# Kernel optimization log

Hardware: AMD Instinct MI355X
Metric: run time of the kernel (lower is better)

## Reference

```python
import jax, jax.numpy as jnp
import numpy as np

TOP_K = 16
NUM_HEADS = 1
EPS = 1e-8  # torch F.cosine_similarity eps


def setup_inputs() -> dict:
    key = jax.random.key(0)
    ks = jax.random.split(key, 8)
    B, N, Dk, Dv = 64, 8192, 256, 256
    return {
        "query": jax.random.normal(ks[0], (B, Dk), jnp.float32),
        "key_memory": jax.random.normal(ks[1], (B, N, Dk), jnp.float32),
        "value_memory": jax.random.normal(ks[2], (B, N, Dv), jnp.float32),
        "iteration": jax.random.randint(ks[3], (B, 1), 0, N),
        "in_proj_w": jax.random.normal(ks[4], (3 * Dv, Dv), jnp.float32) * 0.06,
        "in_proj_b": jnp.zeros((3 * Dv,), jnp.float32),
        "out_proj_w": jax.random.normal(ks[5], (Dv, Dv), jnp.float32) * 0.06,
        "out_proj_b": jnp.zeros((Dv,), jnp.float32),
    }


def _mha(x, in_w, in_b, out_w, out_b):
    # torch nn.MultiheadAttention (batch_first, qkv same embed dim) self-attention
    B, T, E = x.shape
    H = NUM_HEADS
    hd = E // H
    qkv = x @ in_w.T + in_b                      # [B,T,3E]
    q, k, v = jnp.split(qkv, 3, axis=-1)

    def heads(t):
        return t.reshape(B, T, H, hd).transpose(0, 2, 1, 3)  # [B,H,T,hd]

    q, k, v = heads(q), heads(k), heads(v)
    scale = jnp.asarray(1.0 / np.sqrt(hd), x.dtype)
    attn = jax.nn.softmax(jnp.einsum('bhqd,bhkd->bhqk', q, k) * scale, axis=-1)
    o = jnp.einsum('bhqk,bhkd->bhqd', attn, v).transpose(0, 2, 1, 3).reshape(B, T, E)
    return o @ out_w.T + out_b


def reference(query, key_memory, value_memory, iteration,
              in_proj_w, in_proj_b, out_proj_w, out_proj_b):
    B, N, Dv = value_memory.shape
    # memory validity mask: item n is valid iff n <= iteration[b]
    mem_idx = jnp.arange(N)[None, :]                                   # [1,N]
    mask = (mem_idx <= iteration).astype(key_memory.dtype)[..., None]  # [B,N,1]
    km = key_memory * mask
    vm = value_memory * mask

    # masked cosine similarity between each memory key and the query
    num = jnp.einsum('bnd,bd->bn', km, query)                          # [B,N]
    denom = jnp.maximum(
        jnp.linalg.norm(km, axis=-1) * jnp.linalg.norm(query, axis=-1, keepdims=True),
        EPS)
    sim = num / denom                                                  # [B,N]

    topk_sim, topk_idx = jax.lax.top_k(sim, TOP_K)                     # [B,K]
    topk_vm = jnp.take_along_axis(vm, topk_idx[:, :, None], axis=1)    # [B,K,Dv]

    wv = jax.nn.softmax(topk_sim, axis=-1)[..., None]                  # [B,K,1]
    nrv = wv * topk_vm                                                 # [B,K,Dv]

    nrv = _mha(nrv, in_proj_w, in_proj_b, out_proj_w, out_proj_b)      # [B,K,Dv]

    # rows with iteration == 0 are left as zeros (scatter of computed rows)
    not_first = (iteration.reshape(-1) > 0).astype(nrv.dtype)[:, None, None]
    nrv = nrv * not_first
    return nrv.sum(axis=1)                                             # [B,Dv]
```

## Files before the change

### kernel.cpp

```cpp
#include <hip/hip_runtime.h>
#include <hip/hip_bf16.h>
#include <math.h>

#define B_   64
#define N_   8192
#define D_   256
#define K_   16
#define EPS_ 1e-8f
#define NEG_ -3.4e38f

static const size_t CANDV_OFF = 0;
static const size_t CANDI_OFF = 131072;
static const size_t QKV_OFF   = 262144;

__global__ void __launch_bounds__(256)
simtopk_kernel(const float* __restrict__ q, const float* __restrict__ km,
               const int* __restrict__ iter,
               float* __restrict__ cand_v, int* __restrict__ cand_i) {
    int tid  = threadIdx.x;
    int w    = tid >> 6, lane = tid & 63;
    int g    = lane >> 4, p = lane & 15;
    int item = (blockIdx.x << 2) + w;
    int b    = item >> 7;
    int r0   = (item & 127) << 6;
    int it   = iter[b];
    size_t cbase = (size_t)item * K_;

    if (r0 > it) {
        if (lane < K_) { cand_v[cbase + lane] = 0.f; cand_i[cbase + lane] = r0 + lane; }
        return;
    }

    float4 q4[4];
    #pragma unroll
    for (int kk = 0; kk < 4; kk++)
        q4[kk] = *(const float4*)(q + (size_t)b * D_ + kk * 64 + p * 4);
    float qq = 0.f;
    #pragma unroll
    for (int kk = 0; kk < 4; kk++)
        qq += q4[kk].x*q4[kk].x + q4[kk].y*q4[kk].y + q4[kk].z*q4[kk].z + q4[kk].w*q4[kk].w;
    #pragma unroll
    for (int off = 8; off; off >>= 1) qq += __shfl_xor(qq, off);
    float qn = sqrtf(qq);

    float keepv = 0.f;
    const float* kmb = km + (size_t)b * N_ * D_;
    for (int t = 0; t < 8; t++) {
        int ra = r0 + (t << 3) + (g << 1);
        int rb = ra + 1;
        const float* pa = kmb + (size_t)min(ra, it) * D_;
        const float* pb = kmb + (size_t)min(rb, it) * D_;
        float4 ka0 = *(const float4*)(pa +   0 + p * 4);
        float4 ka1 = *(const float4*)(pa +  64 + p * 4);
        float4 ka2 = *(const float4*)(pa + 128 + p * 4);
        float4 ka3 = *(const float4*)(pa + 192 + p * 4);
        float4 kb0 = *(const float4*)(pb +   0 + p * 4);
        float4 kb1 = *(const float4*)(pb +  64 + p * 4);
        float4 kb2 = *(const float4*)(pb + 128 + p * 4);
        float4 kb3 = *(const float4*)(pb + 192 + p * 4);
        float dota = ka0.x*q4[0].x + ka0.y*q4[0].y + ka0.z*q4[0].z + ka0.w*q4[0].w
                   + ka1.x*q4[1].x + ka1.y*q4[1].y + ka1.z*q4[1].z + ka1.w*q4[1].w
                   + ka2.x*q4[2].x + ka2.y*q4[2].y + ka2.z*q4[2].z + ka2.w*q4[2].w
                   + ka3.x*q4[3].x + ka3.y*q4[3].y + ka3.z*q4[3].z + ka3.w*q4[3].w;
        float sqa  = ka0.x*ka0.x + ka0.y*ka0.y + ka0.z*ka0.z + ka0.w*ka0.w
                   + ka1.x*ka1.x + ka1.y*ka1.y + ka1.z*ka1.z + ka1.w*ka1.w
                   + ka2.x*ka2.x + ka2.y*ka2.y + ka2.z*ka2.z + ka2.w*ka2.w
                   + ka3.x*ka3.x + ka3.y*ka3.y + ka3.z*ka3.z + ka3.w*ka3.w;
        float dotb = kb0.x*q4[0].x + kb0.y*q4[0].y + kb0.z*q4[0].z + kb0.w*q4[0].w
                   + kb1.x*q4[1].x + kb1.y*q4[1].y + kb1.z*q4[1].z + kb1.w*q4[1].w
                   + kb2.x*q4[2].x + kb2.y*q4[2].y + kb2.z*q4[2].z + kb2.w*q4[2].w
                   + kb3.x*q4[3].x + kb3.y*q4[3].y + kb3.z*q4[3].z + kb3.w*q4[3].w;
        float sqb  = kb0.x*kb0.x + kb0.y*kb0.y + kb0.z*kb0.z + kb0.w*kb0.w
                   + kb1.x*kb1.x + kb1.y*kb1.y + kb1.z*kb1.z + kb1.w*kb1.w
                   + kb2.x*kb2.x + kb2.y*kb2.y + kb2.z*kb2.z + kb2.w*kb2.w
                   + kb3.x*kb3.x + kb3.y*kb3.y + kb3.z*kb3.z + kb3.w*kb3.w;
        #pragma unroll
        for (int off = 8; off; off >>= 1) {
            dota += __shfl_xor(dota, off);
            sqa  += __shfl_xor(sqa,  off);
            dotb += __shfl_xor(dotb, off);
            sqb  += __shfl_xor(sqb,  off);
        }
        float sa = (ra <= it) ? dota / fmaxf(sqrtf(sqa) * qn, EPS_) : 0.f;
        float sb = (rb <= it) ? dotb / fmaxf(sqrtf(sqb) * qn, EPS_) : 0.f;
        keepv = (p == 2 * t)     ? sa : keepv;
        keepv = (p == 2 * t + 1) ? sb : keepv;
    }
    int keepi = r0 + ((p >> 1) << 3) + (g << 1) + (p & 1);

    #pragma unroll
    for (int k = 2; k <= 64; k <<= 1) {
        #pragma unroll
        for (int j = k >> 1; j > 0; j >>= 1) {
            float pv = __shfl_xor(keepv, j);
            int   pi = __shfl_xor(keepi, j);
            bool up         = ((lane & k) == 0);
            bool is_lower   = ((lane & j) == 0);
            bool mine_first = (keepv > pv) || (keepv == pv && keepi < pi);
            bool take_mine  = ((is_lower == up) == mine_first);
            if (!take_mine) { keepv = pv; keepi = pi; }
        }
    }
    if (lane < K_) { cand_v[cbase + lane] = keepv; cand_i[cbase + lane] = keepi; }
}

__global__ void __launch_bounds__(256)
merge_qkv_kernel(const float* __restrict__ cand_v, const int* __restrict__ cand_i,
                 const float* __restrict__ vm, const int* __restrict__ iter,
                 const float* __restrict__ inw, const float* __restrict__ inb,
                 float* __restrict__ qkv) {
    int bwh = blockIdx.x;
    int b = bwh / 3, which = bwh - b * 3;
    int tid = threadIdx.x, lane = tid & 63;
    int it = iter[b];
    if (it == 0) return;

    __shared__ int   seli[K_];
    __shared__ float selv[K_];
    __shared__ float scl[K_];

    if (tid < 64) {
        float cv[32]; int ci[32];
        #pragma unroll
        for (int j = 0; j < 32; j++) {
            cv[j] = cand_v[(size_t)b * 2048 + (j << 6) + lane];
            ci[j] = cand_i[(size_t)b * 2048 + (j << 6) + lane];
        }
        for (int sel = 0; sel < K_; sel++) {
            float bv = cv[0]; int bi = ci[0];
            #pragma unroll
            for (int j = 1; j < 32; j++)
                if (cv[j] > bv || (cv[j] == bv && ci[j] < bi)) { bv = cv[j]; bi = ci[j]; }
            #pragma unroll
            for (int off = 32; off; off >>= 1) {
                float ov = __shfl_xor(bv, off);
                int   oi = __shfl_xor(bi, off);
                if (ov > bv || (ov == bv && oi < bi)) { bv = ov; bi = oi; }
            }
            #pragma unroll
            for (int j = 0; j < 32; j++)
                if (ci[j] == bi) cv[j] = NEG_;
            if (lane == 0) { selv[sel] = bv; seli[sel] = bi; }
        }
        float m = NEG_;
        #pragma unroll
        for (int jj = 0; jj < K_; jj++) m = fmaxf(m, selv[jj]);
        float ssum = 0.f;
        #pragma unroll
        for (int jj = 0; jj < K_; jj++) ssum += expf(selv[jj] - m);
        if (lane < K_) {
            int row = seli[lane];
            float wgt = expf(selv[lane] - m) / ssum;
            scl[lane] = (row <= it) ? wgt : 0.f;
        }
    }
    __syncthreads();

    float acc[K_];
    #pragma unroll
    for (int k = 0; k < K_; k++) acc[k] = 0.f;
    const float* wrow = inw + (size_t)(which * D_ + tid) * D_;
    for (int blk = 0; blk < 4; blk++) {
        float4 wreg[16];
        #pragma unroll
        for (int u = 0; u < 16; u++)
            wreg[u] = *(const float4*)(wrow + blk * 64 + u * 4);
        #pragma unroll
        for (int k = 0; k < K_; k++) {
            int row = __builtin_amdgcn_readfirstlane(seli[k]);
            const float* vr = vm + ((size_t)b * N_ + row) * D_ + blk * 64;
            float a = 0.f;
            #pragma unroll
            for (int u = 0; u < 16; u++) {
                float4 xv = *(const float4*)(vr + u * 4);
                a += xv.x*wreg[u].x + xv.y*wreg[u].y + xv.z*wreg[u].z + xv.w*wreg[u].w;
            }
            acc[k] += a;
        }
    }
    float bias = inb[which * D_ + tid];
    #pragma unroll
    for (int k = 0; k < K_; k++)
        qkv[(((size_t)b * 3 + which) * K_ + k) * D_ + tid] = scl[k] * acc[k] + bias;
}

__global__ void __launch_bounds__(256)
attn_out_kernel(const float* __restrict__ qkv, const int* __restrict__ iter,
                const float* __restrict__ ow, const float* __restrict__ ob,
                float* __restrict__ out) {
    int b = blockIdx.x, tid = threadIdx.x;
    int it = iter[b];
    if (it == 0) { out[(size_t)b * D_ + tid] = 0.f; return; }
    __shared__ float qs[K_][260];
    __shared__ float ks[K_][260];
    __shared__ float vs[K_][260];
    __shared__ float attn[K_][K_];
    __shared__ float colsum[K_];
    __shared__ float so[D_];
    const float* base = qkv + (size_t)b * 3 * K_ * D_;
    #pragma unroll
    for (int k = 0; k < K_; k++) {
        qs[k][tid] = base[(0 * K_ + k) * D_ + tid];
        ks[k][tid] = base[(1 * K_ + k) * D_ + tid];
        vs[k][tid] = base[(2 * K_ + k) * D_ + tid];
    }
    __syncthreads();
    int i = tid >> 4, j = tid & 15;
    float s = 0.f;
    for (int d4 = 0; d4 < 64; d4++) {
        float4 qv = *(const float4*)(&qs[i][d4 * 4]);
        float4 kv = *(const float4*)(&ks[j][d4 * 4]);
        s += qv.x*kv.x + qv.y*kv.y + qv.z*kv.z + qv.w*kv.w;
    }
    attn[i][j] = s * 0.0625f;
    __syncthreads();
    if (tid < K_) {
        float m = NEG_;
        for (int jj = 0; jj < K_; jj++) m = fmaxf(m, attn[tid][jj]);
        float ssum = 0.f;
        for (int jj = 0; jj < K_; jj++) ssum += expf(attn[tid][jj] - m);
        float inv = 1.f / ssum;
        for (int jj = 0; jj < K_; jj++) attn[tid][jj] = expf(attn[tid][jj] - m) * inv;
    }
    __syncthreads();
    if (tid < K_) {
        float c = 0.f;
        for (int ii = 0; ii < K_; ii++) c += attn[ii][tid];
        colsum[tid] = c;
    }
    __syncthreads();
    float acc = 0.f;
    #pragma unroll
    for (int jj = 0; jj < K_; jj++) acc += colsum[jj] * vs[jj][tid];
    so[tid] = acc;
    __syncthreads();
    float o = 0.f;
    const float* orow = ow + (size_t)tid * D_;
    for (int e = 0; e < D_; e += 4) {
        float4 wv = *(const float4*)(orow + e);
        float4 sv = *(const float4*)(&so[e]);
        o += sv.x*wv.x + sv.y*wv.y + sv.z*wv.z + sv.w*wv.w;
    }
    out[(size_t)b * D_ + tid] = o + 16.f * ob[tid];
}

extern "C" void kernel_launch(void* const* d_in, const int* in_sizes, int n_in,
                              void* d_out, int out_size, void* d_ws, size_t ws_size,
                              hipStream_t stream) {
    const float* q   = (const float*)d_in[0];
    const float* km  = (const float*)d_in[1];
    const float* vm  = (const float*)d_in[2];
    const int*   it  = (const int*)  d_in[3];
    const float* inw = (const float*)d_in[4];
    const float* inb = (const float*)d_in[5];
    const float* ow  = (const float*)d_in[6];
    const float* ob  = (const float*)d_in[7];
    float* out = (float*)d_out;

    float* ws     = (float*)d_ws;
    float* cand_v = ws + CANDV_OFF;
    int*   cand_i = (int*)(ws + CANDI_OFF);
    float* qkv    = ws + QKV_OFF;

    simtopk_kernel<<<dim3(2048), dim3(256), 0, stream>>>(q, km, it, cand_v, cand_i);
    merge_qkv_kernel<<<dim3(B_ * 3), dim3(256), 0, stream>>>(cand_v, cand_i, vm, it, inw, inb, qkv);
    attn_out_kernel<<<dim3(B_), dim3(256), 0, stream>>>(qkv, it, ow, ob, out);
}
```

Before: 158.4 us.

## Split similarity and candidate top-k kernels, prefetch key rows, stage values in LDS

The fused similarity/top-k kernel becomes two kernels. The first computes cosine similarity one row per 16-lane group and software-prefetches the next key row, writing the scores to a workspace buffer. A separate kernel runs the per-segment bitonic sort to pick candidates. The QKV projection now stages the softmax-scaled gathered value rows in shared memory once, so each thread no longer re-reads them from global memory. This adds a kernel launch and a global round-trip of the similarity array, but should reduce redundant value loads and hide key-load latency.

```diff
diff --git a/kernel.cpp b/kernel.cpp
--- a/kernel.cpp
+++ b/kernel.cpp
@@ -9,99 +9,100 @@
 #define EPS_ 1e-8f
 #define NEG_ -3.4e38f
 
-static const size_t CANDV_OFF = 0;
-static const size_t CANDI_OFF = 131072;
-static const size_t QKV_OFF   = 262144;
-
-__global__ void __launch_bounds__(256)
-simtopk_kernel(const float* __restrict__ q, const float* __restrict__ km,
-               const int* __restrict__ iter,
-               float* __restrict__ cand_v, int* __restrict__ cand_i) {
-    int tid  = threadIdx.x;
-    int w    = tid >> 6, lane = tid & 63;
-    int g    = lane >> 4, p = lane & 15;
-    int item = (blockIdx.x << 2) + w;
-    int b    = item >> 7;
-    int r0   = (item & 127) << 6;
-    int it   = iter[b];
-    size_t cbase = (size_t)item * K_;
-
-    if (r0 > it) {
-        if (lane < K_) { cand_v[cbase + lane] = 0.f; cand_i[cbase + lane] = r0 + lane; }
-        return;
-    }
+static const size_t SIM_OFF   = 0;
+static const size_t CANDV_OFF = 524288;
+static const size_t CANDI_OFF = 655360;
+static const size_t QKV_OFF   = 786432;
+
+__global__ void __launch_bounds__(256)
+sim_kernel(const float* __restrict__ q, const float* __restrict__ km,
+           const int* __restrict__ iter, float* __restrict__ sim) {
+    int tid = threadIdx.x;
+    int w = tid >> 6, lane = tid & 63;
+    int g = lane >> 4, p = lane & 15;
+    int seg = (blockIdx.x << 2) + w;
+    int b   = seg >> 7;
+    int n0  = (seg & 127) << 6;
+    int it  = iter[b];
+    float* simb = sim + (size_t)b * N_;
+
+    if (n0 > it) { simb[n0 + lane] = 0.f; return; }
 
     float4 q4[4];
     #pragma unroll
     for (int kk = 0; kk < 4; kk++)
         q4[kk] = *(const float4*)(q + (size_t)b * D_ + kk * 64 + p * 4);
-    float qq = 0.f;
-    #pragma unroll
-    for (int kk = 0; kk < 4; kk++)
-        qq += q4[kk].x*q4[kk].x + q4[kk].y*q4[kk].y + q4[kk].z*q4[kk].z + q4[kk].w*q4[kk].w;
+    float qq = q4[0].x*q4[0].x + q4[0].y*q4[0].y + q4[0].z*q4[0].z + q4[0].w*q4[0].w
+             + q4[1].x*q4[1].x + q4[1].y*q4[1].y + q4[1].z*q4[1].z + q4[1].w*q4[1].w
+             + q4[2].x*q4[2].x + q4[2].y*q4[2].y + q4[2].z*q4[2].z + q4[2].w*q4[2].w
+             + q4[3].x*q4[3].x + q4[3].y*q4[3].y + q4[3].z*q4[3].z + q4[3].w*q4[3].w;
     #pragma unroll
     for (int off = 8; off; off >>= 1) qq += __shfl_xor(qq, off);
     float qn = sqrtf(qq);
 
-    float keepv = 0.f;
     const float* kmb = km + (size_t)b * N_ * D_;
-    for (int t = 0; t < 8; t++) {
-        int ra = r0 + (t << 3) + (g << 1);
-        int rb = ra + 1;
-        const float* pa = kmb + (size_t)min(ra, it) * D_;
-        const float* pb = kmb + (size_t)min(rb, it) * D_;
-        float4 ka0 = *(const float4*)(pa +   0 + p * 4);
-        float4 ka1 = *(const float4*)(pa +  64 + p * 4);
-        float4 ka2 = *(const float4*)(pa + 128 + p * 4);
-        float4 ka3 = *(const float4*)(pa + 192 + p * 4);
-        float4 kb0 = *(const float4*)(pb +   0 + p * 4);
-        float4 kb1 = *(const float4*)(pb +  64 + p * 4);
-        float4 kb2 = *(const float4*)(pb + 128 + p * 4);
-        float4 kb3 = *(const float4*)(pb + 192 + p * 4);
-        float dota = ka0.x*q4[0].x + ka0.y*q4[0].y + ka0.z*q4[0].z + ka0.w*q4[0].w
-                   + ka1.x*q4[1].x + ka1.y*q4[1].y + ka1.z*q4[1].z + ka1.w*q4[1].w
-                   + ka2.x*q4[2].x + ka2.y*q4[2].y + ka2.z*q4[2].z + ka2.w*q4[2].w
-                   + ka3.x*q4[3].x + ka3.y*q4[3].y + ka3.z*q4[3].z + ka3.w*q4[3].w;
-        float sqa  = ka0.x*ka0.x + ka0.y*ka0.y + ka0.z*ka0.z + ka0.w*ka0.w
-                   + ka1.x*ka1.x + ka1.y*ka1.y + ka1.z*ka1.z + ka1.w*ka1.w
-                   + ka2.x*ka2.x + ka2.y*ka2.y + ka2.z*ka2.z + ka2.w*ka2.w
-                   + ka3.x*ka3.x + ka3.y*ka3.y + ka3.z*ka3.z + ka3.w*ka3.w;
-        float dotb = kb0.x*q4[0].x + kb0.y*q4[0].y + kb0.z*q4[0].z + kb0.w*q4[0].w
-                   + kb1.x*q4[1].x + kb1.y*q4[1].y + kb1.z*q4[1].z + kb1.w*q4[1].w
-                   + kb2.x*q4[2].x + kb2.y*q4[2].y + kb2.z*q4[2].z + kb2.w*q4[2].w
-                   + kb3.x*q4[3].x + kb3.y*q4[3].y + kb3.z*q4[3].z + kb3.w*q4[3].w;
-        float sqb  = kb0.x*kb0.x + kb0.y*kb0.y + kb0.z*kb0.z + kb0.w*kb0.w
-                   + kb1.x*kb1.x + kb1.y*kb1.y + kb1.z*kb1.z + kb1.w*kb1.w
-                   + kb2.x*kb2.x + kb2.y*kb2.y + kb2.z*kb2.z + kb2.w*kb2.w
-                   + kb3.x*kb3.x + kb3.y*kb3.y + kb3.z*kb3.z + kb3.w*kb3.w;
+
+    const float* rp0 = kmb + (size_t)min(n0 + g, it) * D_;
+    float4 c0 = *(const float4*)(rp0 +   0 + p * 4);
+    float4 c1 = *(const float4*)(rp0 +  64 + p * 4);
+    float4 c2 = *(const float4*)(rp0 + 128 + p * 4);
+    float4 c3 = *(const float4*)(rp0 + 192 + p * 4);
+
+    for (int t = 0; t < 16; t++) {
+        int r  = n0 + (t << 2) + g;
+        int rn = (t < 15) ? (r + 4) : it;
+        const float* rp = kmb + (size_t)min(rn, it) * D_;
+        float4 x0 = *(const float4*)(rp +   0 + p * 4);
+        float4 x1 = *(const float4*)(rp +  64 + p * 4);
+        float4 x2 = *(const float4*)(rp + 128 + p * 4);
+        float4 x3 = *(const float4*)(rp + 192 + p * 4);
+
+        float dot = c0.x*q4[0].x + c0.y*q4[0].y + c0.z*q4[0].z + c0.w*q4[0].w
+                  + c1.x*q4[1].x + c1.y*q4[1].y + c1.z*q4[1].z + c1.w*q4[1].w
+                  + c2.x*q4[2].x + c2.y*q4[2].y + c2.z*q4[2].z + c2.w*q4[2].w
+                  + c3.x*q4[3].x + c3.y*q4[3].y + c3.z*q4[3].z + c3.w*q4[3].w;
+        float sq  = c0.x*c0.x + c0.y*c0.y + c0.z*c0.z + c0.w*c0.w
+                  + c1.x*c1.x + c1.y*c1.y + c1.z*c1.z + c1.w*c1.w
+                  + c2.x*c2.x + c2.y*c2.y + c2.z*c2.z + c2.w*c2.w
+                  + c3.x*c3.x + c3.y*c3.y + c3.z*c3.z + c3.w*c3.w;
         #pragma unroll
         for (int off = 8; off; off >>= 1) {
-            dota += __shfl_xor(dota, off);
-            sqa  += __shfl_xor(sqa,  off);
-            dotb += __shfl_xor(dotb, off);
-            sqb  += __shfl_xor(sqb,  off);
-        }
-        float sa = (ra <= it) ? dota / fmaxf(sqrtf(sqa) * qn, EPS_) : 0.f;
-        float sb = (rb <= it) ? dotb / fmaxf(sqrtf(sqb) * qn, EPS_) : 0.f;
-        keepv = (p == 2 * t)     ? sa : keepv;
-        keepv = (p == 2 * t + 1) ? sb : keepv;
-    }
-    int keepi = r0 + ((p >> 1) << 3) + (g << 1) + (p & 1);
-
+            dot += __shfl_xor(dot, off);
+            sq  += __shfl_xor(sq,  off);
+        }
+        float s = (r <= it) ? dot / fmaxf(sqrtf(sq) * qn, EPS_) : 0.f;
+        if (p == 0) simb[r] = s;
+        c0 = x0; c1 = x1; c2 = x2; c3 = x3;
+    }
+}
+
+__global__ void __launch_bounds__(256)
+cand_kernel(const float* __restrict__ sim,
+            float* __restrict__ cand_v, int* __restrict__ cand_i) {
+    int tid = threadIdx.x;
+    int w = tid >> 6, lane = tid & 63;
+    int seg = (blockIdx.x << 2) + w;
+    int b   = seg >> 7;
+    int n0  = (seg & 127) << 6;
+    float v  = sim[(size_t)b * N_ + n0 + lane];
+    int  idx = n0 + lane;
     #pragma unroll
     for (int k = 2; k <= 64; k <<= 1) {
         #pragma unroll
         for (int j = k >> 1; j > 0; j >>= 1) {
-            float pv = __shfl_xor(keepv, j);
-            int   pi = __shfl_xor(keepi, j);
+            float pv = __shfl_xor(v, j);
+            int   pi = __shfl_xor(idx, j);
             bool up         = ((lane & k) == 0);
             bool is_lower   = ((lane & j) == 0);
-            bool mine_first = (keepv > pv) || (keepv == pv && keepi < pi);
+            bool mine_first = (v > pv) || (v == pv && idx < pi);
             bool take_mine  = ((is_lower == up) == mine_first);
-            if (!take_mine) { keepv = pv; keepi = pi; }
-        }
-    }
-    if (lane < K_) { cand_v[cbase + lane] = keepv; cand_i[cbase + lane] = keepi; }
+            if (!take_mine) { v = pv; idx = pi; }
+        }
+    }
+    if (lane < K_) {
+        cand_v[(size_t)seg * K_ + lane] = v;
+        cand_i[(size_t)seg * K_ + lane] = idx;
+    }
 }
 
 __global__ void __launch_bounds__(256)
@@ -116,8 +117,8 @@
     if (it == 0) return;
 
     __shared__ int   seli[K_];
-    __shared__ float selv[K_];
     __shared__ float scl[K_];
+    __shared__ float xs[D_][K_];
 
     if (tid < 64) {
         float cv[32]; int ci[32];
@@ -126,6 +127,7 @@
             cv[j] = cand_v[(size_t)b * 2048 + (j << 6) + lane];
             ci[j] = cand_i[(size_t)b * 2048 + (j << 6) + lane];
         }
+        float selv[K_]; int selidx[K_];
         for (int sel = 0; sel < K_; sel++) {
             float bv = cv[0]; int bi = ci[0];
             #pragma unroll
@@ -140,7 +142,8 @@
             #pragma unroll
             for (int j = 0; j < 32; j++)
                 if (ci[j] == bi) cv[j] = NEG_;
-            if (lane == 0) { selv[sel] = bv; seli[sel] = bi; }
+            selv[sel] = bv; selidx[sel] = bi;
+            if (lane == 0) seli[sel] = bi;
         }
         float m = NEG_;
         #pragma unroll
@@ -149,10 +152,20 @@
         #pragma unroll
         for (int jj = 0; jj < K_; jj++) ssum += expf(selv[jj] - m);
         if (lane < K_) {
-            int row = seli[lane];
             float wgt = expf(selv[lane] - m) / ssum;
-            scl[lane] = (row <= it) ? wgt : 0.f;
-        }
+            scl[lane] = (selidx[lane] <= it) ? wgt : 0.f;
+        }
+    }
+    __syncthreads();
+
+    #pragma unroll
+    for (int kk = 0; kk < K_; kk += 4) {
+        float4 px;
+        px.x = scl[kk+0] * vm[((size_t)b * N_ + seli[kk+0]) * D_ + tid];
+        px.y = scl[kk+1] * vm[((size_t)b * N_ + seli[kk+1]) * D_ + tid];
+        px.z = scl[kk+2] * vm[((size_t)b * N_ + seli[kk+2]) * D_ + tid];
+        px.w = scl[kk+3] * vm[((size_t)b * N_ + seli[kk+3]) * D_ + tid];
+        *(float4*)(&xs[tid][kk]) = px;
     }
     __syncthreads();
 
@@ -160,28 +173,26 @@
     #pragma unroll
     for (int k = 0; k < K_; k++) acc[k] = 0.f;
     const float* wrow = inw + (size_t)(which * D_ + tid) * D_;
-    for (int blk = 0; blk < 4; blk++) {
-        float4 wreg[16];
-        #pragma unroll
-        for (int u = 0; u < 16; u++)
-            wreg[u] = *(const float4*)(wrow + blk * 64 + u * 4);
-        #pragma unroll
-        for (int k = 0; k < K_; k++) {
-            int row = __builtin_amdgcn_readfirstlane(seli[k]);
-            const float* vr = vm + ((size_t)b * N_ + row) * D_ + blk * 64;
-            float a = 0.f;
-            #pragma unroll
-            for (int u = 0; u < 16; u++) {
-                float4 xv = *(const float4*)(vr + u * 4);
-                a += xv.x*wreg[u].x + xv.y*wreg[u].y + xv.z*wreg[u].z + xv.w*wreg[u].w;
-            }
-            acc[k] += a;
+    for (int d = 0; d < D_; d += 4) {
+        float4 wv4 = *(const float4*)(wrow + d);
+        float wk[4] = {wv4.x, wv4.y, wv4.z, wv4.w};
+        #pragma unroll
+        for (int dd = 0; dd < 4; dd++) {
+            float wgt = wk[dd];
+            float4 x0 = *(const float4*)(&xs[d + dd][0]);
+            float4 x1 = *(const float4*)(&xs[d + dd][4]);
+            float4 x2 = *(const float4*)(&xs[d + dd][8]);
+            float4 x3 = *(const float4*)(&xs[d + dd][12]);
+            acc[0]  += x0.x * wgt; acc[1]  += x0.y * wgt; acc[2]  += x0.z * wgt; acc[3]  += x0.w * wgt;
+            acc[4]  += x1.x * wgt; acc[5]  += x1.y * wgt; acc[6]  += x1.z * wgt; acc[7]  += x1.w * wgt;
+            acc[8]  += x2.x * wgt; acc[9]  += x2.y * wgt; acc[10] += x2.z * wgt; acc[11] += x2.w * wgt;
+            acc[12] += x3.x * wgt; acc[13] += x3.y * wgt; acc[14] += x3.z * wgt; acc[15] += x3.w * wgt;
         }
     }
     float bias = inb[which * D_ + tid];
     #pragma unroll
     for (int k = 0; k < K_; k++)
-        qkv[(((size_t)b * 3 + which) * K_ + k) * D_ + tid] = scl[k] * acc[k] + bias;
+        qkv[(((size_t)b * 3 + which) * K_ + k) * D_ + tid] = acc[k] + bias;
 }
 
 __global__ void __launch_bounds__(256)
@@ -258,11 +269,13 @@
     float* out = (float*)d_out;
 
     float* ws     = (float*)d_ws;
+    float* sim    = ws + SIM_OFF;
     float* cand_v = ws + CANDV_OFF;
     int*   cand_i = (int*)(ws + CANDI_OFF);
     float* qkv    = ws + QKV_OFF;
 
-    simtopk_kernel<<<dim3(2048), dim3(256), 0, stream>>>(q, km, it, cand_v, cand_i);
+    sim_kernel<<<dim3(2048), dim3(256), 0, stream>>>(q, km, it, sim);
+    cand_kernel<<<dim3(2048), dim3(256), 0, stream>>>(sim, cand_v, cand_i);
     merge_qkv_kernel<<<dim3(B_ * 3), dim3(256), 0, stream>>>(cand_v, cand_i, vm, it, inw, inb, qkv);
     attn_out_kernel<<<dim3(B_), dim3(256), 0, stream>>>(qkv, it, ow, ob, out);
 }
```

New measurement: 132.8 us. -16.2%, faster.

## Fuse merge/QKV projection and attention-output kernels into one 768-thread tail kernel

Applied to the files above, without the earlier changes.

Merges the top-k merge plus QKV projection kernel and the attention/out-projection kernel into one kernel with one block of 768 threads per batch row. The gathered, softmax-scaled value rows are staged in shared memory once and reused by all three projections, instead of each of three blocks rereading them from global memory. Q, K and V stay in shared memory rather than going through a global workspace, which also removes one kernel launch. The cost is only 64 blocks for the tail work where there were 192 before, plus heavier shared-memory use per block, which may hurt latency hiding.

```diff
diff --git a/kernel.cpp b/kernel.cpp
--- a/kernel.cpp
+++ b/kernel.cpp
@@ -11,7 +11,6 @@
 
 static const size_t CANDV_OFF = 0;
 static const size_t CANDI_OFF = 131072;
-static const size_t QKV_OFF   = 262144;
 
 __global__ void __launch_bounds__(256)
 simtopk_kernel(const float* __restrict__ q, const float* __restrict__ km,
@@ -104,20 +103,29 @@
     if (lane < K_) { cand_v[cbase + lane] = keepv; cand_i[cbase + lane] = keepi; }
 }
 
-__global__ void __launch_bounds__(256)
-merge_qkv_kernel(const float* __restrict__ cand_v, const int* __restrict__ cand_i,
-                 const float* __restrict__ vm, const int* __restrict__ iter,
-                 const float* __restrict__ inw, const float* __restrict__ inb,
-                 float* __restrict__ qkv) {
-    int bwh = blockIdx.x;
-    int b = bwh / 3, which = bwh - b * 3;
+__global__ void __launch_bounds__(768)
+tail_kernel(const float* __restrict__ cand_v, const int* __restrict__ cand_i,
+            const float* __restrict__ vm, const int* __restrict__ iter,
+            const float* __restrict__ inw, const float* __restrict__ inb,
+            const float* __restrict__ ow, const float* __restrict__ ob,
+            float* __restrict__ out) {
+    int b = blockIdx.x;
     int tid = threadIdx.x, lane = tid & 63;
     int it = iter[b];
-    if (it == 0) return;
+    if (it == 0) {
+        if (tid < D_) out[(size_t)b * D_ + tid] = 0.f;
+        return;
+    }
 
     __shared__ int   seli[K_];
-    __shared__ float selv[K_];
     __shared__ float scl[K_];
+    __shared__ float xs[D_][K_];
+    __shared__ float qs[K_][260];
+    __shared__ float ks[K_][260];
+    __shared__ float vs[K_][260];
+    __shared__ float attnS[K_][K_];
+    __shared__ float colsum[K_];
+    __shared__ float so[D_];
 
     if (tid < 64) {
         float cv[32]; int ci[32];
@@ -126,6 +134,7 @@
             cv[j] = cand_v[(size_t)b * 2048 + (j << 6) + lane];
             ci[j] = cand_i[(size_t)b * 2048 + (j << 6) + lane];
         }
+        float selv[K_]; int selidx[K_];
         for (int sel = 0; sel < K_; sel++) {
             float bv = cv[0]; int bi = ci[0];
             #pragma unroll
@@ -140,7 +149,8 @@
             #pragma unroll
             for (int j = 0; j < 32; j++)
                 if (ci[j] == bi) cv[j] = NEG_;
-            if (lane == 0) { selv[sel] = bv; seli[sel] = bi; }
+            selv[sel] = bv; selidx[sel] = bi;
+            if (lane == 0) seli[sel] = bi;
         }
         float m = NEG_;
         #pragma unroll
@@ -149,99 +159,98 @@
         #pragma unroll
         for (int jj = 0; jj < K_; jj++) ssum += expf(selv[jj] - m);
         if (lane < K_) {
-            int row = seli[lane];
             float wgt = expf(selv[lane] - m) / ssum;
-            scl[lane] = (row <= it) ? wgt : 0.f;
-        }
-    }
-    __syncthreads();
-
-    float acc[K_];
-    #pragma unroll
-    for (int k = 0; k < K_; k++) acc[k] = 0.f;
-    const float* wrow = inw + (size_t)(which * D_ + tid) * D_;
-    for (int blk = 0; blk < 4; blk++) {
-        float4 wreg[16];
-        #pragma unroll
-        for (int u = 0; u < 16; u++)
-            wreg[u] = *(const float4*)(wrow + blk * 64 + u * 4);
-        #pragma unroll
-        for (int k = 0; k < K_; k++) {
-            int row = __builtin_amdgcn_readfirstlane(seli[k]);
-            const float* vr = vm + ((size_t)b * N_ + row) * D_ + blk * 64;
-            float a = 0.f;
-            #pragma unroll
-            for (int u = 0; u < 16; u++) {
-                float4 xv = *(const float4*)(vr + u * 4);
-                a += xv.x*wreg[u].x + xv.y*wreg[u].y + xv.z*wreg[u].z + xv.w*wreg[u].w;
+            scl[lane] = (selidx[lane] <= it) ? wgt : 0.f;
+        }
+    }
+    __syncthreads();
+
+    if (tid < D_) {
+        #pragma unroll
+        for (int kk = 0; kk < K_; kk += 4) {
+            float4 px;
+            px.x = scl[kk+0] * vm[((size_t)b * N_ + seli[kk+0]) * D_ + tid];
+            px.y = scl[kk+1] * vm[((size_t)b * N_ + seli[kk+1]) * D_ + tid];
+            px.z = scl[kk+2] * vm[((size_t)b * N_ + seli[kk+2]) * D_ + tid];
+            px.w = scl[kk+3] * vm[((size_t)b * N_ + seli[kk+3]) * D_ + tid];
+            *(float4*)(&xs[tid][kk]) = px;
+        }
+    }
+    __syncthreads();
+
+    {
+        int which = tid >> 8, e = tid & 255;
+        float acc[K_];
+        #pragma unroll
+        for (int k = 0; k < K_; k++) acc[k] = 0.f;
+        const float* wrow = inw + (size_t)(which * D_ + e) * D_;
+        for (int d = 0; d < D_; d += 4) {
+            float4 wv4 = *(const float4*)(wrow + d);
+            float wk[4] = {wv4.x, wv4.y, wv4.z, wv4.w};
+            #pragma unroll
+            for (int dd = 0; dd < 4; dd++) {
+                float wgt = wk[dd];
+                float4 x0 = *(const float4*)(&xs[d + dd][0]);
+                float4 x1 = *(const float4*)(&xs[d + dd][4]);
+                float4 x2 = *(const float4*)(&xs[d + dd][8]);
+                float4 x3 = *(const float4*)(&xs[d + dd][12]);
+                acc[0]  += x0.x * wgt; acc[1]  += x0.y * wgt; acc[2]  += x0.z * wgt; acc[3]  += x0.w * wgt;
+                acc[4]  += x1.x * wgt; acc[5]  += x1.y * wgt; acc[6]  += x1.z * wgt; acc[7]  += x1.w * wgt;
+                acc[8]  += x2.x * wgt; acc[9]  += x2.y * wgt; acc[10] += x2.z * wgt; acc[11] += x2.w * wgt;
+                acc[12] += x3.x * wgt; acc[13] += x3.y * wgt; acc[14] += x3.z * wgt; acc[15] += x3.w * wgt;
             }
-            acc[k] += a;
-        }
-    }
-    float bias = inb[which * D_ + tid];
-    #pragma unroll
-    for (int k = 0; k < K_; k++)
-        qkv[(((size_t)b * 3 + which) * K_ + k) * D_ + tid] = scl[k] * acc[k] + bias;
-}
-
-__global__ void __launch_bounds__(256)
-attn_out_kernel(const float* __restrict__ qkv, const int* __restrict__ iter,
-                const float* __restrict__ ow, const float* __restrict__ ob,
-                float* __restrict__ out) {
-    int b = blockIdx.x, tid = threadIdx.x;
-    int it = iter[b];
-    if (it == 0) { out[(size_t)b * D_ + tid] = 0.f; return; }
-    __shared__ float qs[K_][260];
-    __shared__ float ks[K_][260];
-    __shared__ float vs[K_][260];
-    __shared__ float attn[K_][K_];
-    __shared__ float colsum[K_];
-    __shared__ float so[D_];
-    const float* base = qkv + (size_t)b * 3 * K_ * D_;
-    #pragma unroll
-    for (int k = 0; k < K_; k++) {
-        qs[k][tid] = base[(0 * K_ + k) * D_ + tid];
-        ks[k][tid] = base[(1 * K_ + k) * D_ + tid];
-        vs[k][tid] = base[(2 * K_ + k) * D_ + tid];
-    }
-    __syncthreads();
-    int i = tid >> 4, j = tid & 15;
-    float s = 0.f;
-    for (int d4 = 0; d4 < 64; d4++) {
-        float4 qv = *(const float4*)(&qs[i][d4 * 4]);
-        float4 kv = *(const float4*)(&ks[j][d4 * 4]);
-        s += qv.x*kv.x + qv.y*kv.y + qv.z*kv.z + qv.w*kv.w;
-    }
-    attn[i][j] = s * 0.0625f;
+        }
+        float bias = inb[which * D_ + e];
+        float* dst = (which == 0) ? &qs[0][0] : (which == 1) ? &ks[0][0] : &vs[0][0];
+        #pragma unroll
+        for (int k = 0; k < K_; k++)
+            dst[k * 260 + e] = acc[k] + bias;
+    }
+    __syncthreads();
+
+    if (tid < D_) {
+        int i = tid >> 4, j = tid & 15;
+        float s = 0.f;
+        for (int d4 = 0; d4 < 64; d4++) {
+            float4 qv = *(const float4*)(&qs[i][d4 * 4]);
+            float4 kv = *(const float4*)(&ks[j][d4 * 4]);
+            s += qv.x*kv.x + qv.y*kv.y + qv.z*kv.z + qv.w*kv.w;
+        }
+        attnS[i][j] = s * 0.0625f;
+    }
     __syncthreads();
     if (tid < K_) {
         float m = NEG_;
-        for (int jj = 0; jj < K_; jj++) m = fmaxf(m, attn[tid][jj]);
+        for (int jj = 0; jj < K_; jj++) m = fmaxf(m, attnS[tid][jj]);
         float ssum = 0.f;
-        for (int jj = 0; jj < K_; jj++) ssum += expf(attn[tid][jj] - m);
+        for (int jj = 0; jj < K_; jj++) ssum += expf(attnS[tid][jj] - m);
         float inv = 1.f / ssum;
-        for (int jj = 0; jj < K_; jj++) attn[tid][jj] = expf(attn[tid][jj] - m) * inv;
+        for (int jj = 0; jj < K_; jj++) attnS[tid][jj] = expf(attnS[tid][jj] - m) * inv;
     }
     __syncthreads();
     if (tid < K_) {
         float c = 0.f;
-        for (int ii = 0; ii < K_; ii++) c += attn[ii][tid];
+        for (int ii = 0; ii < K_; ii++) c += attnS[ii][tid];
         colsum[tid] = c;
     }
     __syncthreads();
-    float acc = 0.f;
-    #pragma unroll
-    for (int jj = 0; jj < K_; jj++) acc += colsum[jj] * vs[jj][tid];
-    so[tid] = acc;
-    __syncthreads();
-    float o = 0.f;
-    const float* orow = ow + (size_t)tid * D_;
-    for (int e = 0; e < D_; e += 4) {
-        float4 wv = *(const float4*)(orow + e);
-        float4 sv = *(const float4*)(&so[e]);
-        o += sv.x*wv.x + sv.y*wv.y + sv.z*wv.z + sv.w*wv.w;
-    }
-    out[(size_t)b * D_ + tid] = o + 16.f * ob[tid];
+    if (tid < D_) {
+        float acc = 0.f;
+        #pragma unroll
+        for (int jj = 0; jj < K_; jj++) acc += colsum[jj] * vs[jj][tid];
+        so[tid] = acc;
+    }
+    __syncthreads();
+    if (tid < D_) {
+        float o = 0.f;
+        const float* orow = ow + (size_t)tid * D_;
+        for (int e = 0; e < D_; e += 4) {
+            float4 wv = *(const float4*)(orow + e);
+            float4 sv = *(const float4*)(&so[e]);
+            o += sv.x*wv.x + sv.y*wv.y + sv.z*wv.z + sv.w*wv.w;
+        }
+        out[(size_t)b * D_ + tid] = o + 16.f * ob[tid];
+    }
 }
 
 extern "C" void kernel_launch(void* const* d_in, const int* in_sizes, int n_in,
@@ -260,9 +269,7 @@
     float* ws     = (float*)d_ws;
     float* cand_v = ws + CANDV_OFF;
     int*   cand_i = (int*)(ws + CANDI_OFF);
-    float* qkv    = ws + QKV_OFF;
 
     simtopk_kernel<<<dim3(2048), dim3(256), 0, stream>>>(q, km, it, cand_v, cand_i);
-    merge_qkv_kernel<<<dim3(B_ * 3), dim3(256), 0, stream>>>(cand_v, cand_i, vm, it, inw, inb, qkv);
-    attn_out_kernel<<<dim3(B_), dim3(256), 0, stream>>>(qkv, it, ow, ob, out);
+    tail_kernel<<<dim3(B_), dim3(768), 0, stream>>>(cand_v, cand_i, vm, it, inw, inb, ow, ob, out);
 }
```

Measured after the change: 131.8 us. -16.8%, faster.
